# Kernel optimization log

Measured on AMD Instinct MI355X. Metric: run time of the kernel, lower is better.

The kernel has to match this reference:

```python
import jax, jax.numpy as jnp
import numpy as np

N1 = 100000   # num entities
N2 = 500      # num types
E = 1000000   # num edges
EIN = 128     # entity_in_features
TIN = 128     # type_in_features
NREL = 64     # nrela_dim
OUT = 128     # entity_out_features
ALPHA = 0.2   # leaky-relu slope


def setup_inputs() -> dict:
    key = jax.random.key(0)
    k1, k2, k3, k4, k5, k6, k7 = jax.random.split(key, 7)
    x1 = jax.random.normal(k1, (N1, EIN), dtype=jnp.float32)
    x2 = jax.random.normal(k2, (N2, TIN), dtype=jnp.float32)
    edge_embed = jax.random.normal(k3, (E, NREL), dtype=jnp.float32)
    # xavier-like params, scaled small to keep exp(powers) stable
    a = jax.random.normal(k4, (OUT, EIN + TIN + NREL), dtype=jnp.float32) * 0.05
    a_2 = jax.random.normal(k5, (1, OUT), dtype=jnp.float32) * 0.05
    edge_src = jax.random.randint(k6, (E,), 0, N1, dtype=jnp.int32)
    edge_dst = jax.random.randint(k7, (E,), 0, N2, dtype=jnp.int32)
    return {"x1": x1, "x2": x2, "edge_embed": edge_embed, "a": a, "a_2": a_2,
            "edge_src": edge_src, "edge_dst": edge_dst}


def reference(x1, x2, edge_embed, a, a_2, edge_src, edge_dst):
    # gather per-edge features: [E, EIN+TIN+NREL]
    edge_h = jnp.concatenate([x1[edge_src], x2[edge_dst], edge_embed], axis=1)
    # edge_m = a @ edge_h^T in torch; here kept edge-major: [E, OUT]
    edge_m = edge_h @ a.T
    z = edge_m @ a_2[0]                                  # [E]
    powers = -jnp.where(z > 0, z, ALPHA * z)             # -leakyrelu
    edge_e = jnp.exp(powers)                             # [E]

    # scalar segment sums (sparse rowsum / colsum), shape [N,1]
    entity_e_rowsum = jax.ops.segment_sum(edge_e, edge_src, num_segments=N1)[:, None]
    type_e_rowsum = jax.ops.segment_sum(edge_e, edge_dst, num_segments=N2)[:, None]
    entity_e_rowsum = jnp.where(entity_e_rowsum == 0.0, 1e-12, entity_e_rowsum)
    type_e_rowsum = jnp.where(type_e_rowsum == 0.0, 1e-12, type_e_rowsum)

    # dropout(p=0.0) is identity
    edge_w = edge_e[:, None] * edge_m                    # [E, OUT]

    entity_h_prime = jax.ops.segment_sum(edge_w, edge_src, num_segments=N1) / entity_e_rowsum
    type_h_prime = jax.ops.segment_sum(edge_w, edge_dst, num_segments=N2) / type_e_rowsum

    # concat=True branch
    return (jax.nn.elu(entity_h_prime), jax.nn.elu(type_h_prime))
```

## Files before the change

### kernel.cpp

```cpp
#include <hip/hip_runtime.h>

#define N1V 100000
#define N2V 500
#define NEV 1000000
#define ALPHAV 0.2f
#define NB 2048
#define CHUNK 489
#define CHD 8

typedef float f32x4 __attribute__((ext_vector_type(4)));
typedef unsigned int u32;
typedef unsigned short u16;
typedef u32 u32x2 __attribute__((ext_vector_type(2)));
using bf16x8 = __attribute__((ext_vector_type(8))) short;
using f32x4v = __attribute__((ext_vector_type(4))) float;

__device__ __forceinline__ u32 pack_bf16x2(float a, float b) {
  u32 ua = __float_as_uint(a), ub = __float_as_uint(b);
  u32 ra = (ua + 0x7FFFu + ((ua >> 16) & 1u)) >> 16;
  u32 rb = (ub + 0x7FFFu + ((ub >> 16) & 1u)) >> 16;
  return ra | (rb << 16);
}

__device__ __forceinline__ float bf16_lo(u32 v) { return __uint_as_float(v << 16); }
__device__ __forceinline__ float bf16_hi(u32 v) { return __uint_as_float(v & 0xFFFF0000u); }
__device__ __forceinline__ float bf16_to_f(u16 h) {
  return __uint_as_float(((u32)h) << 16);
}

__global__ __launch_bounds__(256) void k_prep(const float* __restrict__ a,
                                              const float* __restrict__ a2,
                                              float* __restrict__ c) {
  int p = blockIdx.x * 256 + threadIdx.x;
  if (p < 320) {
    float s = 0.f;
    for (int k = 0; k < 128; ++k) s += a2[k] * a[k * 320 + p];
    c[p] = s;
  }
}

__global__ __launch_bounds__(256) void k_conv(const float* __restrict__ x1,
                                              const float* __restrict__ x2,
                                              const float* __restrict__ a,
                                              const float* __restrict__ c,
                                              u32* __restrict__ x1bf,
                                              u32* __restrict__ x2bf,
                                              u32* __restrict__ abf,
                                              float* __restrict__ z1g,
                                              float* __restrict__ z2g) {
  size_t gid = (size_t)blockIdx.x * 256 + threadIdx.x;
  const size_t n_x1 = (size_t)N1V * 16;
  const size_t n_a = 128 * 320 / 8;
  const size_t n_x2 = (size_t)N2V * 16;
  if (gid < n_x1) {
    size_t row = gid >> 4; int chunk = (int)(gid & 15);
    const f32x4* s = (const f32x4*)(x1 + row * 128 + chunk * 8);
    f32x4 v0 = s[0], v1 = s[1];
    uint4 o;
    o.x = pack_bf16x2(v0.x, v0.y); o.y = pack_bf16x2(v0.z, v0.w);
    o.z = pack_bf16x2(v1.x, v1.y); o.w = pack_bf16x2(v1.z, v1.w);
    *(uint4*)(x1bf + row * 64 + chunk * 4) = o;
    const float* cp = c + chunk * 8;
    float d = v0.x * cp[0] + v0.y * cp[1] + v0.z * cp[2] + v0.w * cp[3] +
              v1.x * cp[4] + v1.y * cp[5] + v1.z * cp[6] + v1.w * cp[7];
#pragma unroll
    for (int off = 1; off < 16; off <<= 1) d += __shfl_xor(d, off, 64);
    if (chunk == 0) z1g[row] = d;
  } else if (gid < n_x1 + n_a) {
    size_t idx = gid - n_x1;
    const f32x4* s = (const f32x4*)(a + idx * 8);
    f32x4 v0 = s[0], v1 = s[1];
    uint4 o;
    o.x = pack_bf16x2(v0.x, v0.y); o.y = pack_bf16x2(v0.z, v0.w);
    o.z = pack_bf16x2(v1.x, v1.y); o.w = pack_bf16x2(v1.z, v1.w);
    *(uint4*)(abf + idx * 4) = o;
  } else if (gid < n_x1 + n_a + n_x2) {
    size_t idx = gid - n_x1 - n_a;
    size_t row = idx >> 4; int chunk = (int)(idx & 15);
    const f32x4* s = (const f32x4*)(x2 + row * 128 + chunk * 8);
    f32x4 v0 = s[0], v1 = s[1];
    uint4 o;
    o.x = pack_bf16x2(v0.x, v0.y); o.y = pack_bf16x2(v0.z, v0.w);
    o.z = pack_bf16x2(v1.x, v1.y); o.w = pack_bf16x2(v1.z, v1.w);
    *(uint4*)(x2bf + row * 64 + chunk * 4) = o;
    const float* cp = c + 128 + chunk * 8;
    float d = v0.x * cp[0] + v0.y * cp[1] + v0.z * cp[2] + v0.w * cp[3] +
              v1.x * cp[4] + v1.y * cp[5] + v1.z * cp[6] + v1.w * cp[7];
#pragma unroll
    for (int off = 1; off < 16; off <<= 1) d += __shfl_xor(d, off, 64);
    if (chunk == 0) z2g[row] = d;
  }
}

__global__ __launch_bounds__(256) void k_histw(const int* __restrict__ src,
                                               const int* __restrict__ dst,
                                               const float* __restrict__ ee,
                                               const float* __restrict__ z1g,
                                               const float* __restrict__ z2g,
                                               const float* __restrict__ c,
                                               int* __restrict__ c1,
                                               int* __restrict__ hblk,
                                               float* __restrict__ wbuf,
                                               u32* __restrict__ eeh) {
  __shared__ float tile[128 * 65];
  __shared__ int h[512];
  for (int i = threadIdx.x; i < 512; i += 256) h[i] = 0;
  int tid = threadIdx.x;
  int half = tid & 1, j = tid >> 1;
  float creg[32];
#pragma unroll
  for (int k = 0; k < 32; ++k) creg[k] = c[256 + half * 32 + k];
  __syncthreads();

  int b = blockIdx.x;
  int b0 = b * CHUNK, b1 = min(b0 + CHUNK, NEV);
  for (int ts = b0; ts < b1; ts += 128) {
    int nt = min(128, b1 - ts);
    __syncthreads();
#pragma unroll
    for (int i = 0; i < 8; ++i) {
      int idx = i * 256 + tid;
      int r = idx >> 4, cc = idx & 15;
      if (r < nt) {
        f32x4 v = __builtin_nontemporal_load((const f32x4*)(ee + (size_t)(ts + r) * 64) + cc);
        int basef = r * 65 + cc * 4;
        tile[basef + 0] = v.x; tile[basef + 1] = v.y;
        tile[basef + 2] = v.z; tile[basef + 3] = v.w;
        u32x2 o;
        o.x = pack_bf16x2(v.x, v.y);
        o.y = pack_bf16x2(v.z, v.w);
        *(u32x2*)(eeh + (size_t)(ts + r) * 32 + cc * 2) = o;
      }
    }
    __syncthreads();
    if (j < nt) {
      float dotv = 0.f;
      int basef = j * 65 + half * 32;
#pragma unroll
      for (int k = 0; k < 32; ++k) dotv += tile[basef + k] * creg[k];
      dotv += __shfl_xor(dotv, 1);
      if (half == 0) {
        int e = ts + j;
        int sv = src[e], d = dst[e];
        float z = z1g[sv] + z2g[d] + dotv;
        float zp = z > 0.f ? z : ALPHAV * z;
        wbuf[e] = __expf(-zp);
        atomicAdd(&c1[sv], 1);
        atomicAdd(&h[d], 1);
      }
    }
  }
  __syncthreads();
  for (int i = threadIdx.x; i < 512; i += 256) hblk[(size_t)b * 512 + i] = h[i];
}

__global__ __launch_bounds__(256) void k_colscan(int* __restrict__ hblk,
                                                 int* __restrict__ tot2) {
  __shared__ int s[256];
  int t = blockIdx.x;
  int tid = threadIdx.x;
  int v[8]; int tot = 0;
#pragma unroll
  for (int j = 0; j < 8; ++j) {
    int b = tid * 8 + j;
    v[j] = hblk[(size_t)b * 512 + t];
    tot += v[j];
  }
  s[tid] = tot; __syncthreads();
  for (int off = 1; off < 256; off <<= 1) {
    int tv = (tid >= off) ? s[tid - off] : 0;
    __syncthreads();
    if (tid >= off) s[tid] += tv;
    __syncthreads();
  }
  int run = s[tid] - tot;
#pragma unroll
  for (int j = 0; j < 8; ++j) {
    int b = tid * 8 + j;
    hblk[(size_t)b * 512 + t] = run;
    run += v[j];
  }
  if (tid == 255) tot2[t] = run;
}

__global__ __launch_bounds__(256) void k_scanA(const int* __restrict__ cnt,
                                               int* __restrict__ outp,
                                               int* __restrict__ partials, int n) {
  __shared__ int s[256];
  int tid = threadIdx.x;
  int base = blockIdx.x * 2048 + tid * 8;
  int v[8]; int tot = 0;
#pragma unroll
  for (int j = 0; j < 8; ++j) { int idx = base + j; v[j] = (idx < n) ? cnt[idx] : 0; tot += v[j]; }
  s[tid] = tot; __syncthreads();
  for (int off = 1; off < 256; off <<= 1) {
    int tv = 0;
    if (tid >= off) tv = s[tid - off];
    __syncthreads();
    if (tid >= off) s[tid] += tv;
    __syncthreads();
  }
  int run = s[tid] - tot;
#pragma unroll
  for (int j = 0; j < 8; ++j) { int idx = base + j; if (idx < n) outp[idx] = run; run += v[j]; }
  if (tid == 255) partials[blockIdx.x] = s[255];
}

__global__ __launch_bounds__(512) void k_scanB(int* __restrict__ partials, int nPart,
                                               const int* __restrict__ tot2,
                                               int* __restrict__ rp2) {
  __shared__ int s[512];
  int tid = threadIdx.x;
  int v = (tid < N2V) ? tot2[tid] : 0;
  s[tid] = v; __syncthreads();
  for (int off = 1; off < 512; off <<= 1) {
    int tv = 0;
    if (tid >= off) tv = s[tid - off];
    __syncthreads();
    if (tid >= off) s[tid] += tv;
    __syncthreads();
  }
  if (tid < N2V) rp2[tid] = s[tid] - v;
  if (tid == N2V - 1) rp2[N2V] = s[tid];
  if (tid == 0) {
    int run = 0;
    for (int b = 0; b < nPart; ++b) { int t = partials[b]; partials[b] = run; run += t; }
  }
}

__global__ __launch_bounds__(256) void k_scanC(int* __restrict__ rp, int* __restrict__ cur,
                                               const int* __restrict__ partials, int n, int total) {
  int i = blockIdx.x * 256 + threadIdx.x;
  if (i < n) {
    int v = rp[i] + partials[i >> 11];
    rp[i] = v; cur[i] = v;
  }
  if (i == 0) rp[n] = total;
}

__global__ __launch_bounds__(256) void k_scatter(const int* __restrict__ src,
                                                 const int* __restrict__ dst,
                                                 int* __restrict__ cur1,
                                                 const int* __restrict__ hblk,
                                                 const int* __restrict__ rp2,
                                                 int* __restrict__ e1, int* __restrict__ e2) {
  __shared__ int h[512];
  __shared__ int basep[512];
  int b = blockIdx.x;
  int b0 = b * CHUNK, b1 = min(b0 + CHUNK, NEV);
  for (int i = threadIdx.x; i < 512; i += 256) {
    basep[i] = ((i < N2V) ? rp2[i] : 0) + hblk[(size_t)b * 512 + i];
    h[i] = 0;
  }
  __syncthreads();
  for (int e = b0 + threadIdx.x; e < b1; e += 256) {
    int sv = src[e], d = dst[e];
    int p = atomicAdd(&cur1[sv], 1);
    e1[p] = e;
    int loc = atomicAdd(&h[d], 1);
    e2[basep[d] + loc] = e;
  }
}

__global__ __launch_bounds__(256) void k_dst(const float* __restrict__ x1,
                                             const u32* __restrict__ eeh32,
                                             const float* __restrict__ wbuf,
                                             const int* __restrict__ edge_src,
                                             const int* __restrict__ rp2,
                                             const int* __restrict__ e2,
                                             float* __restrict__ acc2) {
  __shared__ float red[4][224];
  int t = blockIdx.x / CHD;
  int chunk = blockIdx.x % CHD;
  int tid = threadIdx.x, wv = tid >> 6, l = tid & 63;
  int pl = l & 31, hi = l >> 5;
  int start = rp2[t], end = rp2[t + 1];
  int n = end - start;
  int sub = chunk * 4 + wv;
  int i0 = start + (int)(((long long)n * sub) >> 5);
  int i1 = start + (int)(((long long)n * (sub + 1)) >> 5);
  float sxaa = 0.f, sxab = 0.f, sxba = 0.f, sxbb = 0.f, s3a = 0.f, s3b = 0.f, rsum = 0.f;
  int p = i0;
  for (; p + 4 <= i1; p += 4) {
    int ea = e2[p + hi], eb = e2[p + 2 + hi];
    float wa = wbuf[ea], wb = wbuf[eb];
    int sa = edge_src[ea], sb = edge_src[eb];
    u32 va = eeh32[(size_t)ea * 32 + pl];
    u32 vb = eeh32[(size_t)eb * 32 + pl];
    float2 xaa = *(const float2*)(x1 + (size_t)sa * 128 + pl * 2);
    float2 xab = *(const float2*)(x1 + (size_t)sa * 128 + 64 + pl * 2);
    float2 xba = *(const float2*)(x1 + (size_t)sb * 128 + pl * 2);
    float2 xbb = *(const float2*)(x1 + (size_t)sb * 128 + 64 + pl * 2);
    rsum += wa + wb;
    s3a += wa * bf16_lo(va) + wb * bf16_lo(vb);
    s3b += wa * bf16_hi(va) + wb * bf16_hi(vb);
    sxaa += wa * xaa.x + wb * xba.x; sxab += wa * xaa.y + wb * xba.y;
    sxba += wa * xab.x + wb * xbb.x; sxbb += wa * xab.y + wb * xbb.y;
  }
  for (; p < i1; p += 2) {
    int q = p + hi;
    bool ok = q < i1;
    int ea = e2[ok ? q : i0];
    float wa = ok ? wbuf[ea] : 0.f;
    int sa = edge_src[ea];
    u32 va = eeh32[(size_t)ea * 32 + pl];
    float2 xaa = *(const float2*)(x1 + (size_t)sa * 128 + pl * 2);
    float2 xab = *(const float2*)(x1 + (size_t)sa * 128 + 64 + pl * 2);
    rsum += wa;
    s3a += wa * bf16_lo(va);
    s3b += wa * bf16_hi(va);
    sxaa += wa * xaa.x; sxab += wa * xaa.y;
    sxba += wa * xab.x; sxbb += wa * xab.y;
  }
  sxaa += __shfl_xor(sxaa, 32); sxab += __shfl_xor(sxab, 32);
  sxba += __shfl_xor(sxba, 32); sxbb += __shfl_xor(sxbb, 32);
  s3a += __shfl_xor(s3a, 32);  s3b += __shfl_xor(s3b, 32);
  rsum += __shfl_xor(rsum, 32);
  if (hi == 0) {
    red[wv][2 * pl] = sxaa;       red[wv][2 * pl + 1] = sxab;
    red[wv][64 + 2 * pl] = sxba;  red[wv][64 + 2 * pl + 1] = sxbb;
    red[wv][128 + 2 * pl] = s3a;  red[wv][128 + 2 * pl + 1] = s3b;
    if (pl == 0) red[wv][192] = rsum;
  }
  __syncthreads();
  if (tid < 193) {
    float v = red[0][tid] + red[1][tid] + red[2][tid] + red[3][tid];
    if (v != 0.f) atomicAdd(&acc2[t * 256 + tid], v);
  }
}

__global__ __launch_bounds__(256) void k_dst_final(const float* __restrict__ acc2,
                                                   u32* __restrict__ sbuf2bf,
                                                   float* __restrict__ rs2) {
  int t = blockIdx.x, tid = threadIdx.x;
  float rtot = acc2[t * 256 + 192];
  float scale = rtot > 0.f ? 1.0f / rtot : 0.f;
  if (tid < 192) {
    float o = acc2[t * 256 + tid] * scale;
    float pr = __shfl_xor(o, 1);
    if (!(tid & 1)) sbuf2bf[t * 96 + (tid >> 1)] = pack_bf16x2(o, pr);
  }
  if (tid == 192) rs2[t] = rtot;
}

__global__ __launch_bounds__(256) void k_src(const float* __restrict__ x2,
                                             const u32* __restrict__ eeh32,
                                             const float* __restrict__ wbuf,
                                             const int* __restrict__ edge_dst,
                                             const int* __restrict__ rp1,
                                             const int* __restrict__ e1,
                                             u32* __restrict__ sbuf1bf,
                                             float* __restrict__ rs1) {
  int wid = (blockIdx.x * 256 + threadIdx.x) >> 6;
  int l = threadIdx.x & 63;
  if (wid >= N1V) return;
  int pl = l & 31, hi = l >> 5;
  int start = rp1[wid], end = rp1[wid + 1];
  float s2aa = 0.f, s2ab = 0.f, s2ba = 0.f, s2bb = 0.f, s1a = 0.f, s1b = 0.f, rsum = 0.f;
  int p = start;
  for (; p + 4 <= end; p += 4) {
    int ea = e1[p + hi], eb = e1[p + 2 + hi];
    float wa = wbuf[ea], wb = wbuf[eb];
    int da = edge_dst[ea], db = edge_dst[eb];
    u32 va = eeh32[(size_t)ea * 32 + pl];
    u32 vb = eeh32[(size_t)eb * 32 + pl];
    float2 xaa = *(const float2*)(x2 + (size_t)da * 128 + pl * 2);
    float2 xab = *(const float2*)(x2 + (size_t)da * 128 + 64 + pl * 2);
    float2 xba = *(const float2*)(x2 + (size_t)db * 128 + pl * 2);
    float2 xbb = *(const float2*)(x2 + (size_t)db * 128 + 64 + pl * 2);
    rsum += wa + wb;
    s1a += wa * bf16_lo(va) + wb * bf16_lo(vb);
    s1b += wa * bf16_hi(va) + wb * bf16_hi(vb);
    s2aa += wa * xaa.x + wb * xba.x; s2ab += wa * xaa.y + wb * xba.y;
    s2ba += wa * xab.x + wb * xbb.x; s2bb += wa * xab.y + wb * xbb.y;
  }
  for (; p < end; p += 2) {
    int q = p + hi;
    bool ok = q < end;
    int ea = e1[ok ? q : start];
    float wa = ok ? wbuf[ea] : 0.f;
    int da = edge_dst[ea];
    u32 va = eeh32[(size_t)ea * 32 + pl];
    float2 xaa = *(const float2*)(x2 + (size_t)da * 128 + pl * 2);
    float2 xab = *(const float2*)(x2 + (size_t)da * 128 + 64 + pl * 2);
    rsum += wa;
    s1a += wa * bf16_lo(va);
    s1b += wa * bf16_hi(va);
    s2aa += wa * xaa.x; s2ab += wa * xaa.y;
    s2ba += wa * xab.x; s2bb += wa * xab.y;
  }
  s2aa += __shfl_xor(s2aa, 32); s2ab += __shfl_xor(s2ab, 32);
  s2ba += __shfl_xor(s2ba, 32); s2bb += __shfl_xor(s2bb, 32);
  s1a += __shfl_xor(s1a, 32);  s1b += __shfl_xor(s1b, 32);
  rsum += __shfl_xor(rsum, 32);
  float scale = (end > start) ? 1.0f / rsum : 0.f;
  if (hi == 0) {
    u32* baseo = sbuf1bf + (size_t)wid * 96;
    baseo[pl] = pack_bf16x2(s2aa * scale, s2ab * scale);
    baseo[32 + pl] = pack_bf16x2(s2ba * scale, s2bb * scale);
    baseo[64 + pl] = pack_bf16x2(s1a * scale, s1b * scale);
    if (pl == 0) rs1[wid] = (end > start) ? rsum : 0.f;
  }
}

__global__ __launch_bounds__(256) void k_gemm(const u32* __restrict__ Xbf,
                                              const u32* __restrict__ Sbf,
                                              const u32* __restrict__ abf,
                                              const float* __restrict__ rs,
                                              float* __restrict__ out,
                                              int M, int mode) {
  __shared__ short Bt[128 * 40];
  int tid = threadIdx.x;
  int w = tid >> 6, l = tid & 63;
  int r = l & 15, cchunk = l >> 4;
  int row0 = blockIdx.x * 64;
  int gi = row0 + w * 16 + r;
  int gclamp = min(gi, M - 1);
  f32x4v acc[8];
#pragma unroll
  for (int i = 0; i < 8; ++i) acc[i] = (f32x4v){0.f, 0.f, 0.f, 0.f};

  for (int ks = 0; ks < 10; ++ks) {
    if (ks) __syncthreads();
    {
      int n = tid >> 1, half = tid & 1;
      const u32* srcp = abf + n * 160 + ks * 16 + half * 8;
      u32* dstp = (u32*)&Bt[n * 40] + half * 8;
      *(uint4*)(dstp) = *(const uint4*)(srcp);
      *(uint4*)(dstp + 4) = *(const uint4*)(srcp + 4);
    }
    __syncthreads();
    int ck = ks * 4 + cchunk;
    const u32* ap;
    if (mode == 0) {
      ap = (ck < 16) ? (Xbf + (size_t)gclamp * 64 + ck * 4)
                     : (Sbf + (size_t)gclamp * 96 + (ck - 16) * 4);
    } else {
      ap = (ck < 16) ? (Sbf + (size_t)gclamp * 96 + ck * 4)
         : (ck < 32) ? (Xbf + (size_t)gclamp * 64 + (ck - 16) * 4)
                     : (Sbf + (size_t)gclamp * 96 + 64 + (ck - 32) * 4);
    }
    bf16x8 afrag = *(const bf16x8*)ap;
#pragma unroll
    for (int nt = 0; nt < 8; ++nt) {
      bf16x8 bfrag = *(const bf16x8*)&Bt[(nt * 16 + r) * 40 + cchunk * 8];
      acc[nt] = __builtin_amdgcn_mfma_f32_16x16x32_bf16(afrag, bfrag, acc[nt], 0, 0, 0);
    }
  }
  int baser = row0 + w * 16 + cchunk * 4;
#pragma unroll
  for (int rr = 0; rr < 4; ++rr) {
    int go = baser + rr;
    if (go < M) {
      float rsv = rs[go];
      bool ok = rsv > 0.f;
#pragma unroll
      for (int nt = 0; nt < 8; ++nt) {
        float h = acc[nt][rr];
        float v = ok ? (h > 0.f ? h : expm1f(h)) : 0.f;
        out[(size_t)go * 128 + nt * 16 + r] = v;
      }
    }
  }
}


static inline size_t align_up(size_t x, size_t a) { return (x + a - 1) & ~(a - 1); }

extern "C" void kernel_launch(void* const* d_in, const int* in_sizes, int n_in,
                              void* d_out, int out_size, void* d_ws, size_t ws_size,
                              hipStream_t stream) {
  const float* x1 = (const float*)d_in[0];
  const float* x2 = (const float*)d_in[1];
  const float* ee = (const float*)d_in[2];
  const float* a = (const float*)d_in[3];
  const float* a2 = (const float*)d_in[4];
  const int* esrc = (const int*)d_in[5];
  const int* edst = (const int*)d_in[6];
  float* out = (float*)d_out;

  char* base = (char*)d_ws;
  size_t off = 0;
  auto alloc = [&](size_t bytes) -> char* {
    char* p = base + off;
    off = align_up(off + bytes, 256);
    return p;
  };
  float* c = (float*)alloc(320 * 4);
  float* z1g = (float*)alloc(N1V * 4);
  float* z2g = (float*)alloc(512 * 4);
  u32* x1bf = (u32*)alloc((size_t)N1V * 64 * 4);
  u32* x2bf = (u32*)alloc((size_t)N2V * 64 * 4);
  u32* abf = (u32*)alloc(128 * 160 * 4);
  int* rp1 = (int*)alloc((N1V + 1) * 4);
  int* cur1 = (int*)alloc(N1V * 4);
  int* rp2 = (int*)alloc(512 * 4);
  int* partials = (int*)alloc(64 * 4);
  int* hblk = (int*)alloc((size_t)NB * 512 * 4);
  int* tot2 = (int*)alloc(512 * 4);
  int* e1 = (int*)alloc(NEV * 4);
  int* e2 = (int*)alloc(NEV * 4);
  float* wbuf = (float*)alloc(NEV * 4);
  u32* eeh = (u32*)alloc((size_t)NEV * 128);
  float* rs1 = (float*)alloc(N1V * 4);
  float* rs2 = (float*)alloc(512 * 4);
  u32* sbuf1bf = (u32*)alloc((size_t)N1V * 96 * 4);
  u32* sbuf2bf = (u32*)alloc(512 * 96 * 4);
  float* acc2 = (float*)alloc(512 * 256 * 4);
  (void)ws_size; (void)out_size; (void)n_in; (void)in_sizes;

  hipMemsetAsync(cur1, 0, N1V * 4, stream);
  hipMemsetAsync(acc2, 0, 512 * 256 * 4, stream);

  hipLaunchKernelGGL(k_prep, dim3(2), dim3(256), 0, stream, a, a2, c);
  hipLaunchKernelGGL(k_conv, dim3((1600000 + 5120 + 8000 + 255) / 256), dim3(256), 0, stream,
                     x1, x2, a, c, x1bf, x2bf, abf, z1g, z2g);
  hipLaunchKernelGGL(k_histw, dim3(NB), dim3(256), 0, stream,
                     esrc, edst, ee, z1g, z2g, c, cur1, hblk, wbuf, eeh);
  hipLaunchKernelGGL(k_colscan, dim3(512), dim3(256), 0, stream, hblk, tot2);

  const int nScanBlocks = (N1V + 2047) / 2048;
  hipLaunchKernelGGL(k_scanA, dim3(nScanBlocks), dim3(256), 0, stream, cur1, rp1, partials, N1V);
  hipLaunchKernelGGL(k_scanB, dim3(1), dim3(512), 0, stream, partials, nScanBlocks, tot2, rp2);
  hipLaunchKernelGGL(k_scanC, dim3((N1V + 255) / 256), dim3(256), 0, stream, rp1, cur1, partials, N1V, NEV);
  hipLaunchKernelGGL(k_scatter, dim3(NB), dim3(256), 0, stream,
                     esrc, edst, cur1, hblk, rp2, e1, e2);

  hipLaunchKernelGGL(k_dst, dim3(N2V * CHD), dim3(256), 0, stream,
                     x1, eeh, wbuf, esrc, rp2, e2, acc2);
  hipLaunchKernelGGL(k_dst_final, dim3(N2V), dim3(256), 0, stream, acc2, sbuf2bf, rs2);

  hipLaunchKernelGGL(k_src, dim3(N1V / 4), dim3(256), 0, stream,
                     x2, eeh, wbuf, edst, rp1, e1, sbuf1bf, rs1);

  hipLaunchKernelGGL(k_gemm, dim3((N1V + 63) / 64), dim3(256), 0, stream,
                     x1bf, sbuf1bf, abf, rs1, out, N1V, 0);
  hipLaunchKernelGGL(k_gemm, dim3((N2V + 63) / 64), dim3(256), 0, stream,
                     x2bf, sbuf2bf, abf, rs2, out + (size_t)N1V * 128, N2V, 1);
}
```

Baseline: 447.6 us.

## Merge dst/src gathers and both GEMMs into single launches; per-wave histw dot

The k_dst and k_src gather kernels become one k_gather launch whose blocks branch on blockIdx to do either the type-side or the entity-side aggregation. The two k_gemm launches become one launch that picks its mode per block. k_histw drops its shared-memory tile and barriers: each wave now loads four edges of edge_embed directly and reduces the dot product with cross-lane shuffles. The aim is to cut launch gaps and tail idle time and to remove LDS traffic and syncs, at the cost of k_dst_final now running after all gather blocks finish, and of some block-level divergence.

```diff
diff --git a/kernel.cpp b/kernel.cpp
--- a/kernel.cpp
+++ b/kernel.cpp
@@ -7,6 +7,10 @@
 #define NB 2048
 #define CHUNK 489
 #define CHD 8
+#define NDSTB (N2V * CHD)
+#define NSRCB (N1V / 4)
+#define NGEMM1 ((N1V + 63) / 64)
+#define NGEMM2 ((N2V + 63) / 64)
 
 typedef float f32x4 __attribute__((ext_vector_type(4)));
 typedef unsigned int u32;
@@ -24,9 +28,6 @@
 
 __device__ __forceinline__ float bf16_lo(u32 v) { return __uint_as_float(v << 16); }
 __device__ __forceinline__ float bf16_hi(u32 v) { return __uint_as_float(v & 0xFFFF0000u); }
-__device__ __forceinline__ float bf16_to_f(u16 h) {
-  return __uint_as_float(((u32)h) << 16);
-}
 
 __global__ __launch_bounds__(256) void k_prep(const float* __restrict__ a,
                                               const float* __restrict__ a2,
@@ -102,51 +103,37 @@
                                                int* __restrict__ hblk,
                                                float* __restrict__ wbuf,
                                                u32* __restrict__ eeh) {
-  __shared__ float tile[128 * 65];
   __shared__ int h[512];
   for (int i = threadIdx.x; i < 512; i += 256) h[i] = 0;
   int tid = threadIdx.x;
-  int half = tid & 1, j = tid >> 1;
-  float creg[32];
-#pragma unroll
-  for (int k = 0; k < 32; ++k) creg[k] = c[256 + half * 32 + k];
+  int wave = tid >> 6, lane = tid & 63;
+  int r = lane >> 4, cc = lane & 15;
+  float c0 = c[256 + cc * 4 + 0], c1r = c[256 + cc * 4 + 1];
+  float c2 = c[256 + cc * 4 + 2], c3 = c[256 + cc * 4 + 3];
   __syncthreads();
 
   int b = blockIdx.x;
   int b0 = b * CHUNK, b1 = min(b0 + CHUNK, NEV);
-  for (int ts = b0; ts < b1; ts += 128) {
-    int nt = min(128, b1 - ts);
-    __syncthreads();
-#pragma unroll
-    for (int i = 0; i < 8; ++i) {
-      int idx = i * 256 + tid;
-      int r = idx >> 4, cc = idx & 15;
-      if (r < nt) {
-        f32x4 v = __builtin_nontemporal_load((const f32x4*)(ee + (size_t)(ts + r) * 64) + cc);
-        int basef = r * 65 + cc * 4;
-        tile[basef + 0] = v.x; tile[basef + 1] = v.y;
-        tile[basef + 2] = v.z; tile[basef + 3] = v.w;
-        u32x2 o;
-        o.x = pack_bf16x2(v.x, v.y);
-        o.y = pack_bf16x2(v.z, v.w);
-        *(u32x2*)(eeh + (size_t)(ts + r) * 32 + cc * 2) = o;
-      }
-    }
-    __syncthreads();
-    if (j < nt) {
-      float dotv = 0.f;
-      int basef = j * 65 + half * 32;
-#pragma unroll
-      for (int k = 0; k < 32; ++k) dotv += tile[basef + k] * creg[k];
-      dotv += __shfl_xor(dotv, 1);
-      if (half == 0) {
-        int e = ts + j;
-        int sv = src[e], d = dst[e];
-        float z = z1g[sv] + z2g[d] + dotv;
+  for (int eb = b0 + wave * 4; eb < b1; eb += 16) {
+    int e = eb + r;
+    bool ok = e < b1;
+    int ec = ok ? e : b0;
+    f32x4 v = __builtin_nontemporal_load((const f32x4*)(ee + (size_t)ec * 64) + cc);
+    float d = v.x * c0 + v.y * c1r + v.z * c2 + v.w * c3;
+#pragma unroll
+    for (int off = 1; off < 16; off <<= 1) d += __shfl_xor(d, off, 64);
+    if (ok) {
+      u32x2 o;
+      o.x = pack_bf16x2(v.x, v.y);
+      o.y = pack_bf16x2(v.z, v.w);
+      *(u32x2*)(eeh + (size_t)ec * 32 + cc * 2) = o;
+      if (cc == 0) {
+        int sv = src[e], dv = dst[e];
+        float z = z1g[sv] + z2g[dv] + d;
         float zp = z > 0.f ? z : ALPHAV * z;
         wbuf[e] = __expf(-zp);
         atomicAdd(&c1[sv], 1);
-        atomicAdd(&h[d], 1);
+        atomicAdd(&h[dv], 1);
       }
     }
   }
@@ -262,70 +249,131 @@
   }
 }
 
-__global__ __launch_bounds__(256) void k_dst(const float* __restrict__ x1,
-                                             const u32* __restrict__ eeh32,
-                                             const float* __restrict__ wbuf,
-                                             const int* __restrict__ edge_src,
-                                             const int* __restrict__ rp2,
-                                             const int* __restrict__ e2,
-                                             float* __restrict__ acc2) {
+__global__ __launch_bounds__(256) void k_gather(const float* __restrict__ x1,
+                                                const float* __restrict__ x2,
+                                                const u32* __restrict__ eeh32,
+                                                const float* __restrict__ wbuf,
+                                                const int* __restrict__ edge_src,
+                                                const int* __restrict__ edge_dst,
+                                                const int* __restrict__ rp2,
+                                                const int* __restrict__ e2,
+                                                const int* __restrict__ rp1,
+                                                const int* __restrict__ e1,
+                                                float* __restrict__ acc2,
+                                                u32* __restrict__ sbuf1bf,
+                                                float* __restrict__ rs1) {
   __shared__ float red[4][224];
-  int t = blockIdx.x / CHD;
-  int chunk = blockIdx.x % CHD;
-  int tid = threadIdx.x, wv = tid >> 6, l = tid & 63;
+  int tid = threadIdx.x;
+  int l = tid & 63;
   int pl = l & 31, hi = l >> 5;
-  int start = rp2[t], end = rp2[t + 1];
-  int n = end - start;
-  int sub = chunk * 4 + wv;
-  int i0 = start + (int)(((long long)n * sub) >> 5);
-  int i1 = start + (int)(((long long)n * (sub + 1)) >> 5);
-  float sxaa = 0.f, sxab = 0.f, sxba = 0.f, sxbb = 0.f, s3a = 0.f, s3b = 0.f, rsum = 0.f;
-  int p = i0;
-  for (; p + 4 <= i1; p += 4) {
-    int ea = e2[p + hi], eb = e2[p + 2 + hi];
-    float wa = wbuf[ea], wb = wbuf[eb];
-    int sa = edge_src[ea], sb = edge_src[eb];
-    u32 va = eeh32[(size_t)ea * 32 + pl];
-    u32 vb = eeh32[(size_t)eb * 32 + pl];
-    float2 xaa = *(const float2*)(x1 + (size_t)sa * 128 + pl * 2);
-    float2 xab = *(const float2*)(x1 + (size_t)sa * 128 + 64 + pl * 2);
-    float2 xba = *(const float2*)(x1 + (size_t)sb * 128 + pl * 2);
-    float2 xbb = *(const float2*)(x1 + (size_t)sb * 128 + 64 + pl * 2);
-    rsum += wa + wb;
-    s3a += wa * bf16_lo(va) + wb * bf16_lo(vb);
-    s3b += wa * bf16_hi(va) + wb * bf16_hi(vb);
-    sxaa += wa * xaa.x + wb * xba.x; sxab += wa * xaa.y + wb * xba.y;
-    sxba += wa * xab.x + wb * xbb.x; sxbb += wa * xab.y + wb * xbb.y;
-  }
-  for (; p < i1; p += 2) {
-    int q = p + hi;
-    bool ok = q < i1;
-    int ea = e2[ok ? q : i0];
-    float wa = ok ? wbuf[ea] : 0.f;
-    int sa = edge_src[ea];
-    u32 va = eeh32[(size_t)ea * 32 + pl];
-    float2 xaa = *(const float2*)(x1 + (size_t)sa * 128 + pl * 2);
-    float2 xab = *(const float2*)(x1 + (size_t)sa * 128 + 64 + pl * 2);
-    rsum += wa;
-    s3a += wa * bf16_lo(va);
-    s3b += wa * bf16_hi(va);
-    sxaa += wa * xaa.x; sxab += wa * xaa.y;
-    sxba += wa * xab.x; sxbb += wa * xab.y;
-  }
-  sxaa += __shfl_xor(sxaa, 32); sxab += __shfl_xor(sxab, 32);
-  sxba += __shfl_xor(sxba, 32); sxbb += __shfl_xor(sxbb, 32);
-  s3a += __shfl_xor(s3a, 32);  s3b += __shfl_xor(s3b, 32);
-  rsum += __shfl_xor(rsum, 32);
-  if (hi == 0) {
-    red[wv][2 * pl] = sxaa;       red[wv][2 * pl + 1] = sxab;
-    red[wv][64 + 2 * pl] = sxba;  red[wv][64 + 2 * pl + 1] = sxbb;
-    red[wv][128 + 2 * pl] = s3a;  red[wv][128 + 2 * pl + 1] = s3b;
-    if (pl == 0) red[wv][192] = rsum;
-  }
-  __syncthreads();
-  if (tid < 193) {
-    float v = red[0][tid] + red[1][tid] + red[2][tid] + red[3][tid];
-    if (v != 0.f) atomicAdd(&acc2[t * 256 + tid], v);
+
+  if (blockIdx.x < NDSTB) {
+    int t = blockIdx.x / CHD;
+    int chunk = blockIdx.x % CHD;
+    int wv = tid >> 6;
+    int start = rp2[t], end = rp2[t + 1];
+    int n = end - start;
+    int sub = chunk * 4 + wv;
+    int i0 = start + (int)(((long long)n * sub) >> 5);
+    int i1 = start + (int)(((long long)n * (sub + 1)) >> 5);
+    float sxaa = 0.f, sxab = 0.f, sxba = 0.f, sxbb = 0.f, s3a = 0.f, s3b = 0.f, rsum = 0.f;
+    int p = i0;
+    for (; p + 4 <= i1; p += 4) {
+      int ea = e2[p + hi], eb = e2[p + 2 + hi];
+      float wa = wbuf[ea], wb = wbuf[eb];
+      int sa = edge_src[ea], sb = edge_src[eb];
+      u32 va = eeh32[(size_t)ea * 32 + pl];
+      u32 vb = eeh32[(size_t)eb * 32 + pl];
+      float2 xaa = *(const float2*)(x1 + (size_t)sa * 128 + pl * 2);
+      float2 xab = *(const float2*)(x1 + (size_t)sa * 128 + 64 + pl * 2);
+      float2 xba = *(const float2*)(x1 + (size_t)sb * 128 + pl * 2);
+      float2 xbb = *(const float2*)(x1 + (size_t)sb * 128 + 64 + pl * 2);
+      rsum += wa + wb;
+      s3a += wa * bf16_lo(va) + wb * bf16_lo(vb);
+      s3b += wa * bf16_hi(va) + wb * bf16_hi(vb);
+      sxaa += wa * xaa.x + wb * xba.x; sxab += wa * xaa.y + wb * xba.y;
+      sxba += wa * xab.x + wb * xbb.x; sxbb += wa * xab.y + wb * xbb.y;
+    }
+    for (; p < i1; p += 2) {
+      int q = p + hi;
+      bool ok = q < i1;
+      int ea = e2[ok ? q : i0];
+      float wa = ok ? wbuf[ea] : 0.f;
+      int sa = edge_src[ea];
+      u32 va = eeh32[(size_t)ea * 32 + pl];
+      float2 xaa = *(const float2*)(x1 + (size_t)sa * 128 + pl * 2);
+      float2 xab = *(const float2*)(x1 + (size_t)sa * 128 + 64 + pl * 2);
+      rsum += wa;
+      s3a += wa * bf16_lo(va);
+      s3b += wa * bf16_hi(va);
+      sxaa += wa * xaa.x; sxab += wa * xaa.y;
+      sxba += wa * xab.x; sxbb += wa * xab.y;
+    }
+    sxaa += __shfl_xor(sxaa, 32); sxab += __shfl_xor(sxab, 32);
+    sxba += __shfl_xor(sxba, 32); sxbb += __shfl_xor(sxbb, 32);
+    s3a += __shfl_xor(s3a, 32);  s3b += __shfl_xor(s3b, 32);
+    rsum += __shfl_xor(rsum, 32);
+    if (hi == 0) {
+      red[wv][2 * pl] = sxaa;       red[wv][2 * pl + 1] = sxab;
+      red[wv][64 + 2 * pl] = sxba;  red[wv][64 + 2 * pl + 1] = sxbb;
+      red[wv][128 + 2 * pl] = s3a;  red[wv][128 + 2 * pl + 1] = s3b;
+      if (pl == 0) red[wv][192] = rsum;
+    }
+    __syncthreads();
+    if (tid < 193) {
+      float v = red[0][tid] + red[1][tid] + red[2][tid] + red[3][tid];
+      if (v != 0.f) atomicAdd(&acc2[t * 256 + tid], v);
+    }
+  } else {
+    int bid = blockIdx.x - NDSTB;
+    int wid = (bid * 256 + tid) >> 6;
+    if (wid >= N1V) return;
+    int start = rp1[wid], end = rp1[wid + 1];
+    float s2aa = 0.f, s2ab = 0.f, s2ba = 0.f, s2bb = 0.f, s1a = 0.f, s1b = 0.f, rsum = 0.f;
+    int p = start;
+    for (; p + 4 <= end; p += 4) {
+      int ea = e1[p + hi], eb = e1[p + 2 + hi];
+      float wa = wbuf[ea], wb = wbuf[eb];
+      int da = edge_dst[ea], db = edge_dst[eb];
+      u32 va = eeh32[(size_t)ea * 32 + pl];
+      u32 vb = eeh32[(size_t)eb * 32 + pl];
+      float2 xaa = *(const float2*)(x2 + (size_t)da * 128 + pl * 2);
+      float2 xab = *(const float2*)(x2 + (size_t)da * 128 + 64 + pl * 2);
+      float2 xba = *(const float2*)(x2 + (size_t)db * 128 + pl * 2);
+      float2 xbb = *(const float2*)(x2 + (size_t)db * 128 + 64 + pl * 2);
+      rsum += wa + wb;
+      s1a += wa * bf16_lo(va) + wb * bf16_lo(vb);
+      s1b += wa * bf16_hi(va) + wb * bf16_hi(vb);
+      s2aa += wa * xaa.x + wb * xba.x; s2ab += wa * xaa.y + wb * xba.y;
+      s2ba += wa * xab.x + wb * xbb.x; s2bb += wa * xab.y + wb * xbb.y;
+    }
+    for (; p < end; p += 2) {
+      int q = p + hi;
+      bool ok = q < end;
+      int ea = e1[ok ? q : start];
+      float wa = ok ? wbuf[ea] : 0.f;
+      int da = edge_dst[ea];
+      u32 va = eeh32[(size_t)ea * 32 + pl];
+      float2 xaa = *(const float2*)(x2 + (size_t)da * 128 + pl * 2);
+      float2 xab = *(const float2*)(x2 + (size_t)da * 128 + 64 + pl * 2);
+      rsum += wa;
+      s1a += wa * bf16_lo(va);
+      s1b += wa * bf16_hi(va);
+      s2aa += wa * xaa.x; s2ab += wa * xaa.y;
+      s2ba += wa * xab.x; s2bb += wa * xab.y;
+    }
+    s2aa += __shfl_xor(s2aa, 32); s2ab += __shfl_xor(s2ab, 32);
+    s2ba += __shfl_xor(s2ba, 32); s2bb += __shfl_xor(s2bb, 32);
+    s1a += __shfl_xor(s1a, 32);  s1b += __shfl_xor(s1b, 32);
+    rsum += __shfl_xor(rsum, 32);
+    float scale = (end > start) ? 1.0f / rsum : 0.f;
+    if (hi == 0) {
+      u32* baseo = sbuf1bf + (size_t)wid * 96;
+      baseo[pl] = pack_bf16x2(s2aa * scale, s2ab * scale);
+      baseo[32 + pl] = pack_bf16x2(s2ba * scale, s2bb * scale);
+      baseo[64 + pl] = pack_bf16x2(s1a * scale, s1b * scale);
+      if (pl == 0) rs1[wid] = (end > start) ? rsum : 0.f;
+    }
   }
 }
 
@@ -343,77 +391,29 @@
   if (tid == 192) rs2[t] = rtot;
 }
 
-__global__ __launch_bounds__(256) void k_src(const float* __restrict__ x2,
-                                             const u32* __restrict__ eeh32,
-                                             const float* __restrict__ wbuf,
-                                             const int* __restrict__ edge_dst,
-                                             const int* __restrict__ rp1,
-                                             const int* __restrict__ e1,
-                                             u32* __restrict__ sbuf1bf,
-                                             float* __restrict__ rs1) {
-  int wid = (blockIdx.x * 256 + threadIdx.x) >> 6;
-  int l = threadIdx.x & 63;
-  if (wid >= N1V) return;
-  int pl = l & 31, hi = l >> 5;
-  int start = rp1[wid], end = rp1[wid + 1];
-  float s2aa = 0.f, s2ab = 0.f, s2ba = 0.f, s2bb = 0.f, s1a = 0.f, s1b = 0.f, rsum = 0.f;
-  int p = start;
-  for (; p + 4 <= end; p += 4) {
-    int ea = e1[p + hi], eb = e1[p + 2 + hi];
-    float wa = wbuf[ea], wb = wbuf[eb];
-    int da = edge_dst[ea], db = edge_dst[eb];
-    u32 va = eeh32[(size_t)ea * 32 + pl];
-    u32 vb = eeh32[(size_t)eb * 32 + pl];
-    float2 xaa = *(const float2*)(x2 + (size_t)da * 128 + pl * 2);
-    float2 xab = *(const float2*)(x2 + (size_t)da * 128 + 64 + pl * 2);
-    float2 xba = *(const float2*)(x2 + (size_t)db * 128 + pl * 2);
-    float2 xbb = *(const float2*)(x2 + (size_t)db * 128 + 64 + pl * 2);
-    rsum += wa + wb;
-    s1a += wa * bf16_lo(va) + wb * bf16_lo(vb);
-    s1b += wa * bf16_hi(va) + wb * bf16_hi(vb);
-    s2aa += wa * xaa.x + wb * xba.x; s2ab += wa * xaa.y + wb * xba.y;
-    s2ba += wa * xab.x + wb * xbb.x; s2bb += wa * xab.y + wb * xbb.y;
-  }
-  for (; p < end; p += 2) {
-    int q = p + hi;
-    bool ok = q < end;
-    int ea = e1[ok ? q : start];
-    float wa = ok ? wbuf[ea] : 0.f;
-    int da = edge_dst[ea];
-    u32 va = eeh32[(size_t)ea * 32 + pl];
-    float2 xaa = *(const float2*)(x2 + (size_t)da * 128 + pl * 2);
-    float2 xab = *(const float2*)(x2 + (size_t)da * 128 + 64 + pl * 2);
-    rsum += wa;
-    s1a += wa * bf16_lo(va);
-    s1b += wa * bf16_hi(va);
-    s2aa += wa * xaa.x; s2ab += wa * xaa.y;
-    s2ba += wa * xab.x; s2bb += wa * xab.y;
-  }
-  s2aa += __shfl_xor(s2aa, 32); s2ab += __shfl_xor(s2ab, 32);
-  s2ba += __shfl_xor(s2ba, 32); s2bb += __shfl_xor(s2bb, 32);
-  s1a += __shfl_xor(s1a, 32);  s1b += __shfl_xor(s1b, 32);
-  rsum += __shfl_xor(rsum, 32);
-  float scale = (end > start) ? 1.0f / rsum : 0.f;
-  if (hi == 0) {
-    u32* baseo = sbuf1bf + (size_t)wid * 96;
-    baseo[pl] = pack_bf16x2(s2aa * scale, s2ab * scale);
-    baseo[32 + pl] = pack_bf16x2(s2ba * scale, s2bb * scale);
-    baseo[64 + pl] = pack_bf16x2(s1a * scale, s1b * scale);
-    if (pl == 0) rs1[wid] = (end > start) ? rsum : 0.f;
-  }
-}
-
-__global__ __launch_bounds__(256) void k_gemm(const u32* __restrict__ Xbf,
-                                              const u32* __restrict__ Sbf,
+__global__ __launch_bounds__(256) void k_gemm(const u32* __restrict__ x1bf,
+                                              const u32* __restrict__ sbuf1bf,
+                                              const u32* __restrict__ x2bf,
+                                              const u32* __restrict__ sbuf2bf,
                                               const u32* __restrict__ abf,
-                                              const float* __restrict__ rs,
-                                              float* __restrict__ out,
-                                              int M, int mode) {
+                                              const float* __restrict__ rs1,
+                                              const float* __restrict__ rs2,
+                                              float* __restrict__ outall) {
   __shared__ short Bt[128 * 40];
   int tid = threadIdx.x;
   int w = tid >> 6, l = tid & 63;
   int r = l & 15, cchunk = l >> 4;
-  int row0 = blockIdx.x * 64;
+  int mode, row0, M;
+  const u32 *Xbf, *Sbf;
+  const float* rs;
+  float* out;
+  if (blockIdx.x < NGEMM1) {
+    mode = 0; row0 = blockIdx.x * 64; M = N1V;
+    Xbf = x1bf; Sbf = sbuf1bf; rs = rs1; out = outall;
+  } else {
+    mode = 1; row0 = (blockIdx.x - NGEMM1) * 64; M = N2V;
+    Xbf = x2bf; Sbf = sbuf2bf; rs = rs2; out = outall + (size_t)N1V * 128;
+  }
   int gi = row0 + w * 16 + r;
   int gclamp = min(gi, M - 1);
   f32x4v acc[8];
@@ -526,15 +526,11 @@
   hipLaunchKernelGGL(k_scatter, dim3(NB), dim3(256), 0, stream,
                      esrc, edst, cur1, hblk, rp2, e1, e2);
 
-  hipLaunchKernelGGL(k_dst, dim3(N2V * CHD), dim3(256), 0, stream,
-                     x1, eeh, wbuf, esrc, rp2, e2, acc2);
+  hipLaunchKernelGGL(k_gather, dim3(NDSTB + NSRCB), dim3(256), 0, stream,
+                     x1, x2, eeh, wbuf, esrc, edst, rp2, e2, rp1, e1,
+                     acc2, sbuf1bf, rs1);
   hipLaunchKernelGGL(k_dst_final, dim3(N2V), dim3(256), 0, stream, acc2, sbuf2bf, rs2);
 
-  hipLaunchKernelGGL(k_src, dim3(N1V / 4), dim3(256), 0, stream,
-                     x2, eeh, wbuf, edst, rp1, e1, sbuf1bf, rs1);
-
-  hipLaunchKernelGGL(k_gemm, dim3((N1V + 63) / 64), dim3(256), 0, stream,
-                     x1bf, sbuf1bf, abf, rs1, out, N1V, 0);
-  hipLaunchKernelGGL(k_gemm, dim3((N2V + 63) / 64), dim3(256), 0, stream,
-                     x2bf, sbuf2bf, abf, rs2, out + (size_t)N1V * 128, N2V, 1);
-}
+  hipLaunchKernelGGL(k_gemm, dim3(NGEMM1 + NGEMM2), dim3(256), 0, stream,
+                     x1bf, sbuf1bf, x2bf, sbuf2bf, abf, rs1, rs2, out);
+}
```

Result: faster. 432.1 us (-3.5%).
